# Optimization experiments

Hardware: AMD Instinct MI355X
Metric: run time of the kernel (lower is better)

## Reference

```python
import jax, jax.numpy as jnp
import numpy as np

B, T, D_IN = 64, 512, 512
D_HID, D_OUT = 1024, 512
NUM_DAYS = 24
EPS = 1e-5


def setup_inputs() -> dict:
    key = jax.random.key(0)
    ks = jax.random.split(key, 8)
    x = jax.random.normal(ks[0], (B, T, D_IN), dtype=jnp.float32)
    day_indices = jax.random.randint(ks[1], (B,), 0, NUM_DAYS)
    s1 = 1.0 / np.sqrt(D_IN)
    s2 = 1.0 / np.sqrt(D_HID)
    W1 = jax.random.uniform(ks[2], (NUM_DAYS, D_IN, D_HID), jnp.float32, -s1, s1)
    b1 = jax.random.uniform(ks[3], (NUM_DAYS, D_HID), jnp.float32, -s1, s1)
    W2 = jax.random.uniform(ks[4], (NUM_DAYS, D_HID, D_OUT), jnp.float32, -s2, s2)
    b2 = jax.random.uniform(ks[5], (NUM_DAYS, D_OUT), jnp.float32, -s2, s2)
    gamma = jnp.ones((NUM_DAYS, D_OUT), jnp.float32)
    beta = jnp.zeros((NUM_DAYS, D_OUT), jnp.float32)
    return {"x": x, "day_indices": day_indices, "W1": W1, "b1": b1,
            "W2": W2, "b2": b2, "gamma": gamma, "beta": beta}


def reference(x, day_indices, W1, b1, W2, b2, gamma, beta):
    # Gather each sample's day-specific adapter params, then one batched pass.
    # Equivalent to the per-day mask/gather/scatter loop in the torch module.
    # Dropout is identity (eval mode).
    W1d = W1[day_indices]                      # [B, D_in, D_hid]
    b1d = b1[day_indices][:, None, :]          # [B, 1, D_hid]
    W2d = W2[day_indices]                      # [B, D_hid, D_out]
    b2d = b2[day_indices][:, None, :]          # [B, 1, D_out]
    h = jax.nn.relu(jnp.einsum('btd,bdh->bth', x, W1d) + b1d)
    y = jnp.einsum('bth,bho->bto', h, W2d) + b2d
    # per-day LayerNorm over last dim
    mean = jnp.mean(y, axis=-1, keepdims=True)
    var = jnp.var(y, axis=-1, keepdims=True)
    y_hat = (y - mean) * jax.lax.rsqrt(var + EPS)
    g = gamma[day_indices][:, None, :]
    bt = beta[day_indices][:, None, :]
    return y_hat * g + bt
```

## Files before the change

### kernel.cpp

```cpp
#include <hip/hip_runtime.h>

#define B_    64
#define T_    512
#define DIN   512
#define DHID  1024
#define DOUT  512
#define NDAYS 24

typedef unsigned short u16;
typedef __bf16 bf16x8 __attribute__((ext_vector_type(8)));
typedef u16    u16x8  __attribute__((ext_vector_type(8)));
typedef float  f32x4  __attribute__((ext_vector_type(4)));

static __device__ __forceinline__ u16 f2bf(float f) {
    union { float f; unsigned u; } v; v.f = f;
    unsigned r = v.u + 0x7FFFu + ((v.u >> 16) & 1u);
    return (u16)(r >> 16);
}
static __device__ __forceinline__ float bf2f(u16 h) {
    union { unsigned u; float f; } v; v.u = ((unsigned)h) << 16;
    return v.f;
}

static __device__ __forceinline__ void gload_lds16(const void* g, void* l) {
    __builtin_amdgcn_global_load_lds(
        (const __attribute__((address_space(1))) void*)g,
        (__attribute__((address_space(3))) void*)l, 16, 0, 0);
}

__global__ __launch_bounds__(256)
void transpose_w(const float* __restrict__ W, u16* __restrict__ WT, int R, int C) {
    __shared__ float t[32][33];
    const int d  = blockIdx.z;
    const int r0 = blockIdx.y * 32, c0 = blockIdx.x * 32;
    const int tx = threadIdx.x, ty = threadIdx.y;
    const float* Wd = W + (size_t)d * R * C;
    u16* WTd = WT + (size_t)d * R * C;
#pragma unroll
    for (int i = 0; i < 4; ++i)
        t[ty + i * 8][tx] = Wd[(size_t)(r0 + ty + i * 8) * C + c0 + tx];
    __syncthreads();
#pragma unroll
    for (int i = 0; i < 4; ++i)
        WTd[(size_t)(c0 + ty + i * 8) * R + r0 + tx] = f2bf(t[tx][ty + i * 8]);
}

__global__ __launch_bounds__(256)
void cvt_bf16(const float* __restrict__ in, u16* __restrict__ outp, int n8) {
    int i = blockIdx.x * 256 + threadIdx.x;
    const int stride = gridDim.x * 256;
    for (; i < n8; i += stride) {
        float4 a = ((const float4*)in)[i * 2];
        float4 b = ((const float4*)in)[i * 2 + 1];
        u16x8 p;
        p[0] = f2bf(a.x); p[1] = f2bf(a.y); p[2] = f2bf(a.z); p[3] = f2bf(a.w);
        p[4] = f2bf(b.x); p[5] = f2bf(b.y); p[6] = f2bf(b.z); p[7] = f2bf(b.w);
        ((u16x8*)outp)[i] = p;
    }
}

template<int MT, int NT, int KT, bool RELU, bool OUT_BF16>
__global__ __launch_bounds__(512, 1)
void gemm8(const u16* __restrict__ Aall,
           const u16* __restrict__ BT,
           const float* __restrict__ bias,
           const int* __restrict__ didx,
           void* __restrict__ Call)
{
    constexpr int GX = MT / 256;
    constexpr int GY = NT / 256;
    constexpr int NWG = GX * GY * B_;
    constexpr int NT_K = KT / 64;
    static_assert(NT_K >= 2 && (NWG % 8) == 0, "geometry");

    constexpr int Q = NWG / 8;
    const int hw = blockIdx.x;
    const int l  = (hw & 7) * Q + (hw >> 3);
    const int bx = l % GX;
    const int by = (l / GX) % GY;
    const int bz = l / (GX * GY);

    const int day = didx[bz];
    const int m0 = bx * 256, n0 = by * 256;
    const int tid = threadIdx.x;
    const int wv = tid >> 6, ln = tid & 63;
    const int wm = wv >> 2, wn = wv & 3;

    __shared__ __align__(16) u16 sA[2][256 * 64];
    __shared__ __align__(16) u16 sB[2][256 * 64];

    const u16* Ab = Aall + (size_t)bz * MT * KT + (size_t)m0 * KT;
    const u16* Bt = BT + (size_t)day * NT * KT + (size_t)n0 * KT;

    auto stageA = [&](int buf, int t, int h) {
#pragma unroll
        for (int c = 0; c < 2; ++c) {
            const int rl = h * 128 + wv * 16 + c * 8 + (ln >> 3);
            const int cd = (ln & 7) ^ (rl & 7);
            gload_lds16(Ab + (size_t)rl * KT + t * 64 + cd * 8,
                        (char*)&sA[buf][(h * 128 + wv * 16 + c * 8) * 64]);
        }
    };
    auto stageB = [&](int buf, int t, int h) {
#pragma unroll
        for (int c = 0; c < 2; ++c) {
            const int rl = h * 128 + wv * 16 + c * 8 + (ln >> 3);
            const int cd = (ln & 7) ^ (rl & 7);
            gload_lds16(Bt + (size_t)rl * KT + t * 64 + cd * 8,
                        (char*)&sB[buf][(h * 128 + wv * 16 + c * 8) * 64]);
        }
    };

    f32x4 acc[8][4];
#pragma unroll
    for (int i = 0; i < 8; ++i)
#pragma unroll
        for (int j = 0; j < 4; ++j)
            acc[i][j] = (f32x4){0.f, 0.f, 0.f, 0.f};

    stageA(0, 0, 0); stageB(0, 0, 0); stageA(0, 0, 1); stageB(0, 0, 1);
    stageA(1, 1, 0); stageB(1, 1, 0);
    asm volatile("s_waitcnt vmcnt(4)" ::: "memory");
    __builtin_amdgcn_s_barrier();

    for (int t = 0; t < NT_K; ++t) {
        const int buf = t & 1;
        const u16* sAb = sA[buf];
        const u16* sBb = sB[buf];
        bf16x8 av[2][4], bv[2][2];

#pragma unroll
        for (int p = 0; p < 4; ++p) {
            const int mq = p >> 1, nq = p & 1;
            if (p == 0 || p == 2) {
#pragma unroll
                for (int ks = 0; ks < 2; ++ks)
#pragma unroll
                    for (int mi = 0; mi < 4; ++mi) {
                        const int r = mq * 128 + wm * 64 + mi * 16 + (ln & 15);
                        const int slot = (ks * 4 + (ln >> 4)) ^ (r & 7);
                        av[ks][mi] = *(const bf16x8*)&sAb[r * 64 + slot * 8];
                    }
            }
#pragma unroll
            for (int ks = 0; ks < 2; ++ks)
#pragma unroll
                for (int ni = 0; ni < 2; ++ni) {
                    const int r = nq * 128 + wn * 32 + ni * 16 + (ln & 15);
                    const int slot = (ks * 4 + (ln >> 4)) ^ (r & 7);
                    bv[ks][ni] = *(const bf16x8*)&sBb[r * 64 + slot * 8];
                }
            if (p == 0)      { if (t + 1 < NT_K) stageA(buf ^ 1, t + 1, 1); }
            else if (p == 1) { if (t + 1 < NT_K) stageB(buf ^ 1, t + 1, 1); }
            else if (p == 2) { if (t + 2 < NT_K) stageA(buf, t + 2, 0); }
            else             { if (t + 2 < NT_K) stageB(buf, t + 2, 0); }

            __builtin_amdgcn_s_barrier();
            asm volatile("s_waitcnt lgkmcnt(0)" ::: "memory");
            __builtin_amdgcn_sched_barrier(0);
            __builtin_amdgcn_s_setprio(1);
#pragma unroll
            for (int ks = 0; ks < 2; ++ks)
#pragma unroll
                for (int mi = 0; mi < 4; ++mi)
#pragma unroll
                    for (int ni = 0; ni < 2; ++ni)
                        acc[mq * 4 + mi][nq * 2 + ni] =
                            __builtin_amdgcn_mfma_f32_16x16x32_bf16(
                                av[ks][mi], bv[ks][ni],
                                acc[mq * 4 + mi][nq * 2 + ni], 0, 0, 0);
            __builtin_amdgcn_s_setprio(0);
            if (p == 3) {
                if (t + 2 < NT_K) asm volatile("s_waitcnt vmcnt(4)" ::: "memory");
                else              asm volatile("s_waitcnt vmcnt(0)" ::: "memory");
            }
            __builtin_amdgcn_s_barrier();
        }
    }

    const float* bs = bias + (size_t)day * NT + n0;
#pragma unroll
    for (int nq = 0; nq < 2; ++nq)
#pragma unroll
        for (int ni = 0; ni < 2; ++ni) {
            const int col = nq * 128 + wn * 32 + ni * 16 + (ln & 15);
            const float bval = bs[col];
#pragma unroll
            for (int mq = 0; mq < 2; ++mq)
#pragma unroll
                for (int mi = 0; mi < 4; ++mi)
#pragma unroll
                    for (int i = 0; i < 4; ++i) {
                        const int row = mq * 128 + wm * 64 + mi * 16 + (ln >> 4) * 4 + i;
                        float v = acc[mq * 4 + mi][nq * 2 + ni][i] + bval;
                        if (RELU) v = fmaxf(v, 0.f);
                        const size_t off = (size_t)bz * MT * NT + (size_t)(m0 + row) * NT + (n0 + col);
                        if (OUT_BF16) ((u16*)Call)[off] = f2bf(v);
                        else          ((float*)Call)[off] = v;
                    }
        }
}

__global__ __launch_bounds__(512, 1)
void gemm2_ln(const u16* __restrict__ Aall,
              const u16* __restrict__ BT,
              const float* __restrict__ bias,
              const int* __restrict__ didx,
              const float* __restrict__ gamma,
              const float* __restrict__ beta,
              float* __restrict__ out)
{
    constexpr int BM = 128, BK = 64;
    constexpr int KT = DHID;
    constexpr int NT_K = KT / BK;
    constexpr int GX = T_ / BM;
    constexpr int NWG = GX * B_;

    constexpr int Q = NWG / 8;
    const int hw = blockIdx.x;
    const int l  = (hw & 7) * Q + (hw >> 3);
    const int bx = l % GX;
    const int bz = l / GX;

    const int day = didx[bz];
    const int m0 = bx * BM;
    const int tid = threadIdx.x;
    const int wv = tid >> 6, ln = tid & 63;
    const int wm = wv >> 2, wn = wv & 3;

    __shared__ __align__(16) u16 sA[2][BM * BK];
    __shared__ __align__(16) u16 sB[2][DOUT * BK];

    const u16* Ab = Aall + (size_t)bz * T_ * KT + (size_t)m0 * KT;
    const u16* Bt = BT + (size_t)day * DOUT * KT;

    auto stageA = [&](int buf, int t) {
#pragma unroll
        for (int c = 0; c < 2; ++c) {
            const int rl = wv * 16 + c * 8 + (ln >> 3);
            const int cd = (ln & 7) ^ (rl & 7);
            gload_lds16(Ab + (size_t)rl * KT + t * BK + cd * 8,
                        (char*)&sA[buf][(wv * 16 + c * 8) * BK]);
        }
    };
    auto stageBh = [&](int buf, int t, int h) {
#pragma unroll
        for (int c = 0; c < 4; ++c) {
            const int rl = h * 256 + wv * 32 + c * 8 + (ln >> 3);
            const int cd = (ln & 7) ^ (rl & 7);
            gload_lds16(Bt + (size_t)rl * KT + t * BK + cd * 8,
                        (char*)&sB[buf][(h * 256 + wv * 32 + c * 8) * BK]);
        }
    };

    f32x4 acc[4][8];
#pragma unroll
    for (int i = 0; i < 4; ++i)
#pragma unroll
        for (int j = 0; j < 8; ++j)
            acc[i][j] = (f32x4){0.f, 0.f, 0.f, 0.f};

    stageA(0, 0); stageBh(0, 0, 0); stageBh(0, 0, 1);
    stageA(1, 1); stageBh(1, 1, 0);
    asm volatile("s_waitcnt vmcnt(6)" ::: "memory");
    __builtin_amdgcn_s_barrier();

    for (int t = 0; t < NT_K; ++t) {
        const int buf = t & 1;
        const u16* sAb = sA[buf];
        const u16* sBb = sB[buf];
        bf16x8 av[2][4], bv[2][2];

#pragma unroll
        for (int p = 0; p < 4; ++p) {
            if (p == 0) {
#pragma unroll
                for (int ks = 0; ks < 2; ++ks)
#pragma unroll
                    for (int mi = 0; mi < 4; ++mi) {
                        const int r = wm * 64 + mi * 16 + (ln & 15);
                        const int slot = (ks * 4 + (ln >> 4)) ^ (r & 7);
                        av[ks][mi] = *(const bf16x8*)&sAb[r * BK + slot * 8];
                    }
            }
#pragma unroll
            for (int ks = 0; ks < 2; ++ks)
#pragma unroll
                for (int ni = 0; ni < 2; ++ni) {
                    const int r = p * 128 + wn * 32 + ni * 16 + (ln & 15);
                    const int slot = (ks * 4 + (ln >> 4)) ^ (r & 7);
                    bv[ks][ni] = *(const bf16x8*)&sBb[r * BK + slot * 8];
                }
            if (p == 0)      { if (t + 1 < NT_K) stageBh(buf ^ 1, t + 1, 1); }
            else if (p == 1) { if (t + 2 < NT_K) stageA(buf, t + 2); }
            else if (p == 2) { if (t + 2 < NT_K) stageBh(buf, t + 2, 0); }

            __builtin_amdgcn_s_barrier();
            asm volatile("s_waitcnt lgkmcnt(0)" ::: "memory");
            __builtin_amdgcn_sched_barrier(0);
            __builtin_amdgcn_s_setprio(1);
#pragma unroll
            for (int ks = 0; ks < 2; ++ks)
#pragma unroll
                for (int mi = 0; mi < 4; ++mi)
#pragma unroll
                    for (int ni = 0; ni < 2; ++ni)
                        acc[mi][p * 2 + ni] =
                            __builtin_amdgcn_mfma_f32_16x16x32_bf16(
                                av[ks][mi], bv[ks][ni], acc[mi][p * 2 + ni], 0, 0, 0);
            __builtin_amdgcn_s_setprio(0);
            if (p == 3) {
                if (t + 2 < NT_K) asm volatile("s_waitcnt vmcnt(6)" ::: "memory");
                else              asm volatile("s_waitcnt vmcnt(0)" ::: "memory");
            }
            __builtin_amdgcn_s_barrier();
        }
    }

    const float* bs = bias + (size_t)day * DOUT;
    float bval[8];
#pragma unroll
    for (int f = 0; f < 8; ++f)
        bval[f] = bs[(f >> 1) * 128 + wn * 32 + (f & 1) * 16 + (ln & 15)];

    u16* yb = (u16*)&sB[0][0];
#pragma unroll
    for (int mi = 0; mi < 4; ++mi)
#pragma unroll
        for (int f = 0; f < 8; ++f) {
            const int col = (f >> 1) * 128 + wn * 32 + (f & 1) * 16 + (ln & 15);
#pragma unroll
            for (int i = 0; i < 4; ++i) {
                const int rloc = wm * 64 + mi * 16 + (ln >> 4) * 4 + i;
                yb[rloc * DOUT + col] = f2bf(acc[mi][f][i] + bval[f]);
            }
        }
    __syncthreads();

    const float* gs = gamma + (size_t)day * DOUT;
    const float* es = beta + (size_t)day * DOUT;
    const float4 g0 = ((const float4*)gs)[ln * 2];
    const float4 g1 = ((const float4*)gs)[ln * 2 + 1];
    const float4 e0 = ((const float4*)es)[ln * 2];
    const float4 e1 = ((const float4*)es)[ln * 2 + 1];

    float* op = out + (size_t)bz * T_ * DOUT + (size_t)m0 * DOUT;
#pragma unroll 4
    for (int r = wv * 16; r < wv * 16 + 16; ++r) {
        const u16x8 yv = *(const u16x8*)&yb[r * DOUT + ln * 8];
        float yf[8];
#pragma unroll
        for (int j = 0; j < 8; ++j) yf[j] = bf2f(yv[j]);
        float s = 0.f, q = 0.f;
#pragma unroll
        for (int j = 0; j < 8; ++j) { s += yf[j]; q += yf[j] * yf[j]; }
#pragma unroll
        for (int o = 32; o; o >>= 1) { s += __shfl_xor(s, o); q += __shfl_xor(q, o); }
        const float mean = s * (1.f / 512.f);
        const float var  = q * (1.f / 512.f) - mean * mean;
        const float rstd = rsqrtf(var + 1e-5f);
        float4 o0, o1;
        o0.x = (yf[0] - mean) * rstd * g0.x + e0.x;
        o0.y = (yf[1] - mean) * rstd * g0.y + e0.y;
        o0.z = (yf[2] - mean) * rstd * g0.z + e0.z;
        o0.w = (yf[3] - mean) * rstd * g0.w + e0.w;
        o1.x = (yf[4] - mean) * rstd * g1.x + e1.x;
        o1.y = (yf[5] - mean) * rstd * g1.y + e1.y;
        o1.z = (yf[6] - mean) * rstd * g1.z + e1.z;
        o1.w = (yf[7] - mean) * rstd * g1.w + e1.w;
        ((float4*)(op + (size_t)r * DOUT))[ln * 2] = o0;
        ((float4*)(op + (size_t)r * DOUT))[ln * 2 + 1] = o1;
    }
}

extern "C" void kernel_launch(void* const* d_in, const int* in_sizes, int n_in,
                              void* d_out, int out_size, void* d_ws, size_t ws_size,
                              hipStream_t stream)
{
    const float* x     = (const float*)d_in[0];
    const int*   didx  = (const int*)d_in[1];
    const float* W1    = (const float*)d_in[2];
    const float* b1    = (const float*)d_in[3];
    const float* W2    = (const float*)d_in[4];
    const float* b2    = (const float*)d_in[5];
    const float* gamma = (const float*)d_in[6];
    const float* beta  = (const float*)d_in[7];
    float* out = (float*)d_out;

    char* ws = (char*)d_ws;
    u16* W1T = (u16*)ws;
    u16* h   = (u16*)(ws + 25165824);
    u16* xb  = (u16*)(ws + 92274688);
    u16* W2T = xb;

    transpose_w<<<dim3(DHID / 32, DIN / 32, NDAYS), dim3(32, 8), 0, stream>>>(W1, W1T, DIN, DHID);
    cvt_bf16<<<2048, 256, 0, stream>>>(x, xb, B_ * T_ * DIN / 8);

    gemm8<T_, DHID, DIN, true, true>
        <<<dim3(2 * 4 * B_), 512, 0, stream>>>(xb, W1T, b1, didx, h);

    transpose_w<<<dim3(DOUT / 32, DHID / 32, NDAYS), dim3(32, 8), 0, stream>>>(W2, W2T, DHID, DOUT);

    gemm2_ln<<<dim3(4 * B_), 512, 0, stream>>>(h, W2T, b2, didx, gamma, beta, out);
}
```

Measured before the change: 155.8 us.

## Fuse weight transposes and input conversion into one prep kernel; reuse fragments in GEMM

```diff
diff --git a/kernel.cpp b/kernel.cpp
--- a/kernel.cpp
+++ b/kernel.cpp
@@ -46,16 +46,45 @@
 }
 
 __global__ __launch_bounds__(256)
-void cvt_bf16(const float* __restrict__ in, u16* __restrict__ outp, int n8) {
-    int i = blockIdx.x * 256 + threadIdx.x;
-    const int stride = gridDim.x * 256;
-    for (; i < n8; i += stride) {
-        float4 a = ((const float4*)in)[i * 2];
-        float4 b = ((const float4*)in)[i * 2 + 1];
-        u16x8 p;
-        p[0] = f2bf(a.x); p[1] = f2bf(a.y); p[2] = f2bf(a.z); p[3] = f2bf(a.w);
-        p[4] = f2bf(b.x); p[5] = f2bf(b.y); p[6] = f2bf(b.z); p[7] = f2bf(b.w);
-        ((u16x8*)outp)[i] = p;
+void aux_prep(const float* __restrict__ W1, u16* __restrict__ W1T,
+              const float* __restrict__ W2, u16* __restrict__ W2T,
+              const float* __restrict__ x, u16* __restrict__ xb,
+              int nW2)
+{
+    __shared__ float t[32][33];
+    const int jb = blockIdx.x;
+    const int tid = threadIdx.x;
+    if (jb < 12288 + nW2) {
+        const float* W; u16* WT; int R, C, j;
+        if (jb < 12288) { W = W1; WT = W1T; R = DIN;  C = DHID; j = jb; }
+        else            { W = W2; WT = W2T; R = DHID; C = DOUT; j = jb - 12288; }
+        const int gx = C / 32, gy = R / 32;
+        const int bx = j % gx;
+        const int by = (j / gx) % gy;
+        const int d  = j / (gx * gy);
+        const int tx = tid & 31, ty = tid >> 5;
+        const float* Wd = W + (size_t)d * R * C;
+        u16* WTd = WT + (size_t)d * R * C;
+#pragma unroll
+        for (int i = 0; i < 4; ++i)
+            t[ty + i * 8][tx] = Wd[(size_t)(by * 32 + ty + i * 8) * C + bx * 32 + tx];
+        __syncthreads();
+#pragma unroll
+        for (int i = 0; i < 4; ++i)
+            WTd[(size_t)(bx * 32 + ty + i * 8) * R + by * 32 + tx] = f2bf(t[tx][ty + i * 8]);
+    } else {
+        const int n8 = B_ * T_ * DIN / 8;
+        const int ncvt = gridDim.x - 12288 - nW2;
+        int i = (jb - 12288 - nW2) * 256 + tid;
+        const int stride = ncvt * 256;
+        for (; i < n8; i += stride) {
+            float4 a = ((const float4*)x)[i * 2];
+            float4 b = ((const float4*)x)[i * 2 + 1];
+            u16x8 p;
+            p[0] = f2bf(a.x); p[1] = f2bf(a.y); p[2] = f2bf(a.z); p[3] = f2bf(a.w);
+            p[4] = f2bf(b.x); p[5] = f2bf(b.y); p[6] = f2bf(b.z); p[7] = f2bf(b.w);
+            ((u16x8*)xb)[i] = p;
+        }
     }
 }
 
@@ -127,38 +156,29 @@
         const int buf = t & 1;
         const u16* sAb = sA[buf];
         const u16* sBb = sB[buf];
-        bf16x8 av[2][4], bv[2][2];
-
-#pragma unroll
-        for (int p = 0; p < 4; ++p) {
-            const int mq = p >> 1, nq = p & 1;
-            if (p == 0 || p == 2) {
-#pragma unroll
-                for (int ks = 0; ks < 2; ++ks)
-#pragma unroll
-                    for (int mi = 0; mi < 4; ++mi) {
-                        const int r = mq * 128 + wm * 64 + mi * 16 + (ln & 15);
-                        const int slot = (ks * 4 + (ln >> 4)) ^ (r & 7);
-                        av[ks][mi] = *(const bf16x8*)&sAb[r * 64 + slot * 8];
-                    }
-            }
+        bf16x8 av0[2][4], av1[2][4], bv0[2][2], bv1[2][2];
+
+        auto readAv = [&](bf16x8 (&dst)[2][4], int mq) {
+#pragma unroll
+            for (int ks = 0; ks < 2; ++ks)
+#pragma unroll
+                for (int mi = 0; mi < 4; ++mi) {
+                    const int r = mq * 128 + wm * 64 + mi * 16 + (ln & 15);
+                    const int slot = (ks * 4 + (ln >> 4)) ^ (r & 7);
+                    dst[ks][mi] = *(const bf16x8*)&sAb[r * 64 + slot * 8];
+                }
+        };
+        auto readBv = [&](bf16x8 (&dst)[2][2], int nq) {
 #pragma unroll
             for (int ks = 0; ks < 2; ++ks)
 #pragma unroll
                 for (int ni = 0; ni < 2; ++ni) {
                     const int r = nq * 128 + wn * 32 + ni * 16 + (ln & 15);
                     const int slot = (ks * 4 + (ln >> 4)) ^ (r & 7);
-                    bv[ks][ni] = *(const bf16x8*)&sBb[r * 64 + slot * 8];
+                    dst[ks][ni] = *(const bf16x8*)&sBb[r * 64 + slot * 8];
                 }
-            if (p == 0)      { if (t + 1 < NT_K) stageA(buf ^ 1, t + 1, 1); }
-            else if (p == 1) { if (t + 1 < NT_K) stageB(buf ^ 1, t + 1, 1); }
-            else if (p == 2) { if (t + 2 < NT_K) stageA(buf, t + 2, 0); }
-            else             { if (t + 2 < NT_K) stageB(buf, t + 2, 0); }
-
-            __builtin_amdgcn_s_barrier();
-            asm volatile("s_waitcnt lgkmcnt(0)" ::: "memory");
-            __builtin_amdgcn_sched_barrier(0);
-            __builtin_amdgcn_s_setprio(1);
+        };
+        auto mfmaQ = [&](bf16x8 (&a)[2][4], bf16x8 (&b)[2][2], int mq, int nq) {
 #pragma unroll
             for (int ks = 0; ks < 2; ++ks)
 #pragma unroll
@@ -167,15 +187,50 @@
                     for (int ni = 0; ni < 2; ++ni)
                         acc[mq * 4 + mi][nq * 2 + ni] =
                             __builtin_amdgcn_mfma_f32_16x16x32_bf16(
-                                av[ks][mi], bv[ks][ni],
+                                a[ks][mi], b[ks][ni],
                                 acc[mq * 4 + mi][nq * 2 + ni], 0, 0, 0);
-            __builtin_amdgcn_s_setprio(0);
-            if (p == 3) {
-                if (t + 2 < NT_K) asm volatile("s_waitcnt vmcnt(4)" ::: "memory");
-                else              asm volatile("s_waitcnt vmcnt(0)" ::: "memory");
-            }
-            __builtin_amdgcn_s_barrier();
-        }
+        };
+
+        readAv(av0, 0); readBv(bv0, 0);
+        if (t + 1 < NT_K) stageA(buf ^ 1, t + 1, 1);
+        __builtin_amdgcn_s_barrier();
+        asm volatile("s_waitcnt lgkmcnt(0)" ::: "memory");
+        __builtin_amdgcn_sched_barrier(0);
+        __builtin_amdgcn_s_setprio(1);
+        mfmaQ(av0, bv0, 0, 0);
+        __builtin_amdgcn_s_setprio(0);
+        __builtin_amdgcn_s_barrier();
+
+        readAv(av1, 1);
+        if (t + 1 < NT_K) stageB(buf ^ 1, t + 1, 1);
+        __builtin_amdgcn_s_barrier();
+        asm volatile("s_waitcnt lgkmcnt(0)" ::: "memory");
+        __builtin_amdgcn_sched_barrier(0);
+        __builtin_amdgcn_s_setprio(1);
+        mfmaQ(av1, bv0, 1, 0);
+        __builtin_amdgcn_s_setprio(0);
+        __builtin_amdgcn_s_barrier();
+
+        readBv(bv1, 1);
+        if (t + 2 < NT_K) stageA(buf, t + 2, 0);
+        __builtin_amdgcn_s_barrier();
+        asm volatile("s_waitcnt lgkmcnt(0)" ::: "memory");
+        __builtin_amdgcn_sched_barrier(0);
+        __builtin_amdgcn_s_setprio(1);
+        mfmaQ(av1, bv1, 1, 1);
+        __builtin_amdgcn_s_setprio(0);
+        __builtin_amdgcn_s_barrier();
+
+        if (t + 2 < NT_K) stageB(buf, t + 2, 0);
+        __builtin_amdgcn_s_barrier();
+        asm volatile("s_waitcnt lgkmcnt(0)" ::: "memory");
+        __builtin_amdgcn_sched_barrier(0);
+        __builtin_amdgcn_s_setprio(1);
+        mfmaQ(av0, bv1, 0, 1);
+        __builtin_amdgcn_s_setprio(0);
+        if (t + 2 < NT_K) asm volatile("s_waitcnt vmcnt(4)" ::: "memory");
+        else              asm volatile("s_waitcnt vmcnt(0)" ::: "memory");
+        __builtin_amdgcn_s_barrier();
     }
 
     const float* bs = bias + (size_t)day * NT + n0;
@@ -391,15 +446,21 @@
     u16* W1T = (u16*)ws;
     u16* h   = (u16*)(ws + 25165824);
     u16* xb  = (u16*)(ws + 92274688);
-    u16* W2T = xb;
-
-    transpose_w<<<dim3(DHID / 32, DIN / 32, NDAYS), dim3(32, 8), 0, stream>>>(W1, W1T, DIN, DHID);
-    cvt_bf16<<<2048, 256, 0, stream>>>(x, xb, B_ * T_ * DIN / 8);
-
-    gemm8<T_, DHID, DIN, true, true>
-        <<<dim3(2 * 4 * B_), 512, 0, stream>>>(xb, W1T, b1, didx, h);
-
-    transpose_w<<<dim3(DOUT / 32, DHID / 32, NDAYS), dim3(32, 8), 0, stream>>>(W2, W2T, DHID, DOUT);
-
-    gemm2_ln<<<dim3(4 * B_), 512, 0, stream>>>(h, W2T, b2, didx, gamma, beta, out);
-}
+
+    const bool bigws = ws_size >= 150994944ULL;
+
+    if (bigws) {
+        u16* W2T = (u16*)(ws + 125829120);
+        aux_prep<<<26624, 256, 0, stream>>>(W1, W1T, W2, W2T, x, xb, 12288);
+        gemm8<T_, DHID, DIN, true, true>
+            <<<dim3(2 * 4 * B_), 512, 0, stream>>>(xb, W1T, b1, didx, h);
+        gemm2_ln<<<dim3(4 * B_), 512, 0, stream>>>(h, W2T, b2, didx, gamma, beta, out);
+    } else {
+        u16* W2T = xb;
+        aux_prep<<<14336, 256, 0, stream>>>(W1, W1T, W2, W2T, x, xb, 0);
+        gemm8<T_, DHID, DIN, true, true>
+            <<<dim3(2 * 4 * B_), 512, 0, stream>>>(xb, W1T, b1, didx, h);
+        transpose_w<<<dim3(DOUT / 32, DHID / 32, NDAYS), dim3(32, 8), 0, stream>>>(W2, W2T, DHID, DOUT);
+        gemm2_ln<<<dim3(4 * B_), 512, 0, stream>>>(h, W2T, b2, didx, gamma, beta, out);
+    }
+}
```

After: 148.9 us. -4.4%, faster.
